# Performance work log

Hardware: AMD Instinct MI355X
Metric: run time of the kernel (lower is better)

The kernel has to match this reference:

```python
import jax, jax.numpy as jnp
import numpy as np
from jax import lax

N = 31      # perfect binary tree, root = node 0, children of i are 2i+1, 2i+2
CH = 10     # hidden channels (out_channel)
S = 8       # hidden spatial size = h_list // 4


def conv3d(x, w, b=None, pad=1):
    out = lax.conv_general_dilated(
        x, w, window_strides=(1, 1, 1), padding=[(pad, pad)] * 3,
        dimension_numbers=('NCDHW', 'OIDHW', 'NCDHW'))
    if b is not None:
        out = out + b[None, :, None, None, None]
    return out


def maxpool2(x):
    return lax.reduce_window(x, -jnp.inf, lax.max, (1, 1, 2, 2, 2), (1, 1, 2, 2, 2), 'VALID')


def up2(x):  # nearest-neighbor upsample x2 on D,H,W
    return jnp.repeat(jnp.repeat(jnp.repeat(x, 2, axis=2), 2, axis=3), 2, axis=4)


def setup_inputs() -> dict:
    key = jax.random.key(0)
    ks = iter(jax.random.split(key, 32))
    r = lambda shape, s=0.1: jax.random.normal(next(ks), shape, dtype=jnp.float32) * s
    inp = {
        'data': jax.random.normal(next(ks), (N, 1, 32, 32, 32), dtype=jnp.float32),
        'h0': jnp.zeros((N, CH, S, S, S), jnp.float32),
        'c0': jnp.zeros((N, CH, S, S, S), jnp.float32),
        'e1a_w': r((16, 1, 3, 3, 3)), 'e1a_b': jnp.zeros((16,), jnp.float32),
        'e1b_w': r((16, 16, 3, 3, 3)), 'e1b_b': jnp.zeros((16,), jnp.float32),
        'e2a_w': r((32, 16, 3, 3, 3)), 'e2a_b': jnp.zeros((32,), jnp.float32),
        'e2b_w': r((20, 32, 3, 3, 3)), 'e2b_b': jnp.zeros((20,), jnp.float32),
        'd2a_w': r((20, 30, 3, 3, 3)), 'd2a_b': jnp.zeros((20,), jnp.float32),
        'd2b_w': r((32, 20, 3, 3, 3)), 'd2b_b': jnp.zeros((32,), jnp.float32),
        'd1a_w': r((16, 48, 3, 3, 3)), 'd1a_b': jnp.zeros((16,), jnp.float32),
        'd1b_w': r((16, 16, 3, 3, 3)), 'd1b_b': jnp.zeros((16,), jnp.float32),
        'd1c_w': r((1, 16, 1, 1, 1)), 'd1c_b': jnp.zeros((1,), jnp.float32),
        'w_iou': r((30, 20, 3, 3, 3)),
        'u_iou': r((30, 10, 3, 3, 3)),
        'u_f': r((10, 10, 3, 3, 3)),
        'b_iou': jnp.zeros((30, S, S, S), jnp.float32),
    }
    return inp


def reference(data, h0, c0, e1a_w, e1a_b, e1b_w, e1b_b, e2a_w, e2a_b, e2b_w, e2b_b,
              d2a_w, d2a_b, d2b_w, d2b_b, d1a_w, d1a_b, d1b_w, d1b_b, d1c_w, d1c_b,
              w_iou, u_iou, u_f, b_iou):
    relu = jax.nn.relu
    # ---- Encoder ----
    x0 = relu(conv3d(relu(conv3d(data, e1a_w, e1a_b)), e1b_w, e1b_b))   # [N,16,32,32,32]
    x = maxpool2(x0)
    x1 = relu(conv3d(relu(conv3d(x, e2a_w, e2a_b)), e2b_w, e2b_b))      # [N,20,16,16,16]
    x = maxpool2(x1)                                                    # [N,20,8,8,8]
    Wx = conv3d(x, w_iou)                                               # [N,30,8,8,8]

    h_all = jnp.zeros((N, CH, S, S, S), Wx.dtype)
    c_all = jnp.zeros((N, CH, S, S, S), Wx.dtype)

    def apply_node(iou, c_in):
        i, o, u = jnp.split(iou + b_iou, 3, axis=1)
        c = jax.nn.sigmoid(i) * jnp.tanh(u) + c_in
        h = jax.nn.sigmoid(o) * jnp.tanh(c)
        return h, c

    # ---- leaves (no children): iou = W_iou(x), c term = initial c0 ----
    leaf = np.arange(N // 2, N)
    h, c = apply_node(Wx[leaf], c0[leaf])
    h_all = h_all.at[leaf].set(h)
    c_all = c_all.at[leaf].set(c)

    # ---- internal levels, bottom-up (topological propagation) ----
    depth = int(np.log2(N + 1))  # 5
    for lvl in range(depth - 2, -1, -1):
        idx = np.arange(2 ** lvl - 1, 2 ** (lvl + 1) - 1)
        ch = np.stack([2 * idx + 1, 2 * idx + 2], axis=1)  # [P,2] children indices
        P = idx.shape[0]
        h_ch = h_all[ch]                                   # [P,2,CH,S,S,S]
        c_ch = c_all[ch]
        h_sum = h_ch.sum(axis=1)
        f = jax.nn.sigmoid(conv3d(h_ch.reshape(P * 2, CH, S, S, S), u_f)).reshape(h_ch.shape)
        c_red = (f * c_ch).sum(axis=1)
        iou = conv3d(h_sum, u_iou)  # NOTE: overwrites W_iou(x) for internal nodes (as in source)
        h, c = apply_node(iou, c_red)
        h_all = h_all.at[idx].set(h)
        c_all = c_all.at[idx].set(c)

    # ---- Decoder (Dropout = identity in eval) ----
    y = up2(h_all)                      # [N,10,16,16,16]
    y = jnp.concatenate([y, x1], axis=1)  # 30 ch
    y = relu(conv3d(y, d2a_w, d2a_b))
    y = relu(conv3d(y, d2b_w, d2b_b))   # 32 ch
    y = up2(y)
    y = jnp.concatenate([y, x0], axis=1)  # 48 ch
    y = relu(conv3d(y, d1a_w, d1a_b))
    y = relu(conv3d(y, d1b_w, d1b_b))
    y = conv3d(y, d1c_w, d1c_b, pad=0)  # [N,1,32,32,32]
    return y
```

## Files before the change

### kernel.cpp

```cpp
#include <hip/hip_runtime.h>
#include <math.h>

typedef _Float16 h2 __attribute__((ext_vector_type(2)));
typedef _Float16 half4_t __attribute__((ext_vector_type(4)));
typedef float f32x4 __attribute__((ext_vector_type(4)));

__device__ inline h2 uph(unsigned u) { return __builtin_bit_cast(h2, u); }
__device__ inline unsigned pkh(float a, float b) {
    return __builtin_bit_cast(unsigned, __builtin_amdgcn_cvt_pkrtz(a, b));
}
__device__ inline float sigf(float x) { return 1.f / (1.f + expf(-x)); }

__global__ __launch_bounds__(256) void repackw(
    const float* __restrict__ src, _Float16* __restrict__ dst,
    int CIw, int CO, int NCH, int total)
{
    int t = blockIdx.x * 256 + threadIdx.x;
    if (t >= total) return;
    int cip = t & 15, co = (t >> 4) & 15, r = t >> 8;
    int tap = r % 27, rc = r / 27;
    int chunk = rc % NCH, slab = rc / NCH;
    int slot_l = ((cip >> 2) - (co >> 2)) & 3;
    int gci = chunk * 16 + slot_l * 4 + (cip & 3);
    int gco = slab * 16 + co;
    float v = 0.f;
    if (gci < CIw && gco < CO) v = src[((size_t)gco * CIw + gci) * 27 + tap];
    dst[t] = (_Float16)v;
}

template<int NCH, int UPP, int UP2, int S2, int CO, int CO2, int D, bool FUSE>
__global__ __launch_bounds__(256) void conv3m(
    const _Float16* __restrict__ up, const _Float16* __restrict__ src,
    const _Float16* __restrict__ bwg, const float* __restrict__ bias,
    _Float16* __restrict__ out, const float* __restrict__ w1c,
    const float* __restrict__ b1c, float* __restrict__ out32)
{
    constexpr int ROWS = (D == 32) ? 10 : 18;
    constexpr int COLS = (D == 32) ? 34 : 18;
    constexpr int DH   = D / 2;
    constexpr int NG   = 3 * ROWS * COLS * 2;
    constexpr int ITERS = (NG + 255) / 256;

    __shared__ __align__(16) _Float16 win[3 * ROWS * COLS * 16];
    __shared__ __align__(16) _Float16 bw[6912];

    const int tid  = threadIdx.x;
    const int lane = tid & 63;
    const int wv   = tid >> 6;
    const int l16  = lane & 15;
    const int quad = lane >> 4;

    int n, d, h0;
    if (D == 32) { h0 = (blockIdx.x & 3) * 8; d = (blockIdx.x >> 2) & 31; n = blockIdx.x >> 7; }
    else         { h0 = 0; d = blockIdx.x & 15; n = blockIdx.x >> 4; }

    const int slab = blockIdx.y;
    const int cob  = slab * 16;
    const int co   = cob + l16;

    size_t baseU[ITERS], baseS[ITERS];
    int dA[ITERS], dB[ITERS];
    bool vld[ITERS];
#pragma unroll
    for (int it = 0; it < ITERS; ++it) {
        int t = tid + it * 256;
        vld[it] = false; dA[it] = 0; dB[it] = 0; baseU[it] = 0; baseS[it] = 0;
        if (t < NG) {
            int g   = t & 1;
            int idx = t >> 1;
            int cc  = idx % COLS;
            int rr  = idx / COLS;
            int hh  = rr % ROWS;
            int dp  = rr / ROWS;
            int zd = d - 1 + dp, zh = h0 + hh - 1, zw = cc - 1;
            vld[it] = (unsigned)zd < (unsigned)D && (unsigned)zh < (unsigned)D &&
                      (unsigned)zw < (unsigned)D;
            int rot  = (cc >> 2) & 3;
            int cell = (rr * COLS + cc) * 16;
            dA[it] = cell + (((2 * g + rot) & 3) << 2);
            dB[it] = cell + (((2 * g + 1 + rot) & 3) << 2);
            if (vld[it]) {
                if (UPP > 0)
                    baseU[it] = ((((size_t)n * DH + (zd >> 1)) * DH + (zh >> 1)) * DH
                                 + (zw >> 1)) * UP2 + g * 8;
                baseS[it] = ((((size_t)n * D + zd) * D + zh) * D + zw) * S2 + g * 8;
            }
        }
    }

    f32x4 acc[4];
    {
        float b0 = (co < CO) ? bias[co] : 0.f;
#pragma unroll
        for (int i = 0; i < 4; ++i) acc[i] = f32x4{b0, b0, b0, b0};
    }

    const int brot = ((quad + (l16 >> 2)) & 3) << 2;

    uint4 preA[ITERS];
    uint4 preB[4];

    auto loadA = [&](int cib) {
        const int cb = cib * 16;
        const bool isup = (UPP > 0) && (cb < UPP);
#pragma unroll
        for (int it = 0; it < ITERS; ++it) {
            int t = tid + it * 256;
            uint4 v = uint4{0u, 0u, 0u, 0u};
            if (t < NG && vld[it]) {
                const _Float16* pp = isup ? (up + baseU[it] + cb)
                                          : (src + baseS[it] + (cb - UPP));
                v = *(const uint4*)pp;
            }
            preA[it] = v;
        }
    };
    auto loadB = [&](int cib) {
        const uint4* bsrc = (const uint4*)(bwg + (size_t)(slab * NCH + cib) * 6912);
#pragma unroll
        for (int it = 0; it < 4; ++it) {
            int t = tid + it * 256;
            preB[it] = (t < 864) ? bsrc[t] : uint4{0u, 0u, 0u, 0u};
        }
    };

    loadA(0);
    loadB(0);

#pragma unroll
    for (int cib = 0; cib < NCH; ++cib) {
        if (cib) __syncthreads();
#pragma unroll
        for (int it = 0; it < 4; ++it) {
            int t = tid + it * 256;
            if (t < 864) ((uint4*)bw)[t] = preB[it];
        }
#pragma unroll
        for (int it = 0; it < ITERS; ++it) {
            int t = tid + it * 256;
            if (t < NG) {
                *(uint2*)&win[dA[it]] = make_uint2(preA[it].x, preA[it].y);
                *(uint2*)&win[dB[it]] = make_uint2(preA[it].z, preA[it].w);
            }
        }
        if (cib + 1 < NCH) { loadA(cib + 1); loadB(cib + 1); }
        __syncthreads();

#pragma unroll
        for (int kd = 0; kd < 3; ++kd) {
#pragma unroll
            for (int kw = 0; kw < 3; ++kw) {
                half4_t bf[3];
#pragma unroll
                for (int kh = 0; kh < 3; ++kh)
                    bf[kh] = *(const half4_t*)&bw[((kd * 3 + kh) * 3 + kw) * 256 + l16 * 16 + brot];
                if (D == 32) {
                    half4_t af[2][4];
#pragma unroll
                    for (int p = 0; p < 2; ++p) {
                        const int ww = p * 16 + l16 + kw;
                        const int arot = ((quad + (ww >> 2)) & 3) << 2;
#pragma unroll
                        for (int rr = 0; rr < 4; ++rr) {
                            const int row = kd * ROWS + wv * 2 + rr;
                            af[p][rr] = *(const half4_t*)&win[(row * COLS + ww) * 16 + arot];
                        }
                    }
#pragma unroll
                    for (int kh = 0; kh < 3; ++kh)
#pragma unroll
                        for (int i = 0; i < 4; ++i)
                            acc[i] = __builtin_amdgcn_mfma_f32_16x16x16f16(
                                af[i & 1][(i >> 1) + kh], bf[kh], acc[i], 0, 0, 0);
                } else {
                    half4_t af[6];
                    const int ww = l16 + kw;
                    const int arot = ((quad + (ww >> 2)) & 3) << 2;
#pragma unroll
                    for (int rr = 0; rr < 6; ++rr) {
                        const int row = kd * ROWS + wv * 4 + rr;
                        af[rr] = *(const half4_t*)&win[(row * COLS + ww) * 16 + arot];
                    }
#pragma unroll
                    for (int kh = 0; kh < 3; ++kh)
#pragma unroll
                        for (int i = 0; i < 4; ++i)
                            acc[i] = __builtin_amdgcn_mfma_f32_16x16x16f16(
                                af[i + kh], bf[kh], acc[i], 0, 0, 0);
                }
            }
        }
    }

    if (FUSE) {
        const float wc = w1c[l16];
        const float bb = b1c[0];
#pragma unroll
        for (int i = 0; i < 4; ++i) {
            const int h = h0 + wv * 2 + (i >> 1);
            const int wb0 = (i & 1) * 16;
#pragma unroll
            for (int r = 0; r < 4; ++r) {
                float v = fmaxf(acc[i][r], 0.f) * wc;
                v += __shfl_xor(v, 1);
                v += __shfl_xor(v, 2);
                v += __shfl_xor(v, 4);
                v += __shfl_xor(v, 8);
                if (l16 == 0) {
                    const int w = wb0 + quad * 4 + r;
                    out32[(((size_t)n * 32 + d) * 32 + h) * 32 + w] = v + bb;
                }
            }
        }
    } else if (co < CO) {
#pragma unroll
        for (int i = 0; i < 4; ++i) {
            int h, wb0;
            if (D == 32) { h = h0 + wv * 2 + (i >> 1); wb0 = (i & 1) * 16; }
            else         { h = wv * 4 + i;             wb0 = 0; }
#pragma unroll
            for (int r = 0; r < 4; ++r) {
                const int w = wb0 + quad * 4 + r;
                size_t sp = (((size_t)n * D + d) * D + h) * D + w;
                out[sp * CO2 + co] = (_Float16)fmaxf(acc[i][r], 0.f);
            }
        }
    }
}

__global__ __launch_bounds__(256) void conv3e1a(
    const float* __restrict__ src, const float* __restrict__ wgt,
    const float* __restrict__ bias, _Float16* __restrict__ out)
{
    __shared__ float sw[27 * 16];
    const int tid = threadIdx.x;
    const int wq = tid % 8;
    const int h  = (tid / 8) % 32;
    const int w0 = wq * 4;
    const int n  = blockIdx.x / 32;
    const int d  = blockIdx.x % 32;

    for (int t = tid; t < 27 * 16; t += 256) {
        int co = t % 16, tap = t / 16;
        sw[t] = wgt[(size_t)co * 27 + tap];
    }
    __syncthreads();

    float acc[16][4];
#pragma unroll
    for (int co = 0; co < 16; ++co) {
        float b0 = bias[co];
        acc[co][0] = b0; acc[co][1] = b0; acc[co][2] = b0; acc[co][3] = b0;
    }

#pragma unroll
    for (int kd = 0; kd < 3; ++kd) {
        int zd = d + kd - 1;
        if ((unsigned)zd >= 32u) continue;
#pragma unroll
        for (int kh = 0; kh < 3; ++kh) {
            int zh = h + kh - 1;
            if ((unsigned)zh >= 32u) continue;
            const float* p = src + ((size_t)n * 32 + zd) * 1024 + zh * 32;
            float v[6];
#pragma unroll
            for (int j = 0; j < 6; ++j) {
                int zw = w0 - 1 + j;
                v[j] = ((unsigned)zw < 32u) ? p[zw] : 0.f;
            }
            const float* swp = &sw[(kd * 9 + kh * 3) * 16];
#pragma unroll
            for (int kw = 0; kw < 3; ++kw)
#pragma unroll
                for (int co = 0; co < 16; ++co)
#pragma unroll
                    for (int j = 0; j < 4; ++j)
                        acc[co][j] = fmaf(v[kw + j], swp[kw * 16 + co], acc[co][j]);
        }
    }

#pragma unroll
    for (int j = 0; j < 4; ++j) {
        unsigned u[8];
#pragma unroll
        for (int cp = 0; cp < 8; ++cp)
            u[cp] = pkh(fmaxf(acc[2 * cp][j], 0.f), fmaxf(acc[2 * cp + 1][j], 0.f));
        _Float16* base = out + ((((size_t)n * 32 + d) * 32 + h) * 32 + (w0 + j)) * 16;
        *(uint4*)base       = make_uint4(u[0], u[1], u[2], u[3]);
        *(uint4*)(base + 8) = make_uint4(u[4], u[5], u[6], u[7]);
    }
}

__global__ __launch_bounds__(256) void maxpool16(
    const unsigned* __restrict__ in, unsigned* __restrict__ out, int total)
{
    int t = blockIdx.x * 256 + threadIdx.x;
    if (t >= total) return;
    int cp = t & 7, w = (t >> 3) & 15, h = (t >> 7) & 15, d = (t >> 11) & 15, n = t >> 15;
    float m0 = -1e30f, m1 = -1e30f;
#pragma unroll
    for (int a = 0; a < 2; ++a)
#pragma unroll
        for (int b = 0; b < 2; ++b)
#pragma unroll
            for (int c = 0; c < 2; ++c) {
                size_t sp = (((size_t)n * 32 + 2 * d + a) * 32 + 2 * h + b) * 32 + 2 * w + c;
                h2 x = uph(in[sp * 8 + cp]);
                m0 = fmaxf(m0, (float)x.x);
                m1 = fmaxf(m1, (float)x.y);
            }
    out[(((size_t)(n * 16 + d) * 16 + h) * 16 + w) * 8 + cp] = pkh(m0, m1);
}

__global__ __launch_bounds__(256) void poolx1(
    const unsigned* __restrict__ x1u, unsigned* __restrict__ out, int total)
{
    int t = blockIdx.x * 256 + threadIdx.x;
    if (t >= total) return;
    int cp = t & 15, s = (t >> 4) & 511, n = t >> 13;
    int w = s & 7, h = (s >> 3) & 7, d = s >> 6;
    unsigned o = 0u;
    if (cp < 10) {
        float m0 = -1e30f, m1 = -1e30f;
#pragma unroll
        for (int a = 0; a < 2; ++a)
#pragma unroll
            for (int b = 0; b < 2; ++b)
#pragma unroll
                for (int c = 0; c < 2; ++c) {
                    size_t sp = (((size_t)n * 16 + 2 * d + a) * 16 + 2 * h + b) * 16 + 2 * w + c;
                    h2 x = uph(x1u[sp * 16 + cp]);
                    m0 = fmaxf(m0, (float)x.x);
                    m1 = fmaxf(m1, (float)x.y);
                }
        o = pkh(m0, m1);
    }
    out[((size_t)n * 512 + s) * 16 + cp] = o;
}

__global__ __launch_bounds__(256) void catk(
    const unsigned* __restrict__ h_allu, const unsigned* __restrict__ x1u,
    unsigned* __restrict__ cat1u, int total)
{
    int t = blockIdx.x * 256 + threadIdx.x;
    if (t >= total) return;
    int cp = t & 15, ww = (t >> 4) & 15, hh = (t >> 8) & 15, dd = (t >> 12) & 15, n = t >> 16;
    unsigned v = 0u;
    if (cp < 5) {
        int sph = (dd >> 1) * 64 + (hh >> 1) * 8 + (ww >> 1);
        v = h_allu[((size_t)n * 512 + sph) * 8 + cp];
    } else if (cp < 15) {
        v = x1u[((((size_t)n * 16 + dd) * 16 + hh) * 16 + ww) * 16 + (cp - 5)];
    }
    cat1u[t] = v;
}

__global__ __launch_bounds__(256) void treeleafM(
    const _Float16* __restrict__ xp2, const _Float16* __restrict__ bwio,
    const float* __restrict__ b_iou, const float* __restrict__ c0,
    _Float16* __restrict__ h_all, _Float16* __restrict__ c_all)
{
    __shared__ __align__(16) _Float16 buf[16384];
    __shared__ __align__(16) _Float16 bw[13824];
    const int tid = threadIdx.x, lane = tid & 63, wv = tid >> 6;
    const int l16 = lane & 15, quad = lane >> 4;
    const int node = 15 + blockIdx.x;
    const _Float16* xb = xp2 + (size_t)node * 512 * 32;
    const int brot = ((quad + (l16 >> 2)) & 3) << 2;

    int base[8];
#pragma unroll
    for (int i = 0; i < 8; ++i) {
        int s = (wv * 8 + i) * 16 + l16;
        base[i] = ((s >> 6) * 10 + ((s >> 3) & 7)) * 10 + (s & 7);
    }

    f32x4 acc[2][8];
#pragma unroll
    for (int sl = 0; sl < 2; ++sl)
#pragma unroll
        for (int i = 0; i < 8; ++i) acc[sl][i] = f32x4{0.f, 0.f, 0.f, 0.f};

    for (int ck = 0; ck < 2; ++ck) {
        if (ck) __syncthreads();
        {
            const uint4* s0 = (const uint4*)(bwio + (size_t)(0 * 2 + ck) * 6912);
            const uint4* s1 = (const uint4*)(bwio + (size_t)(1 * 2 + ck) * 6912);
#pragma unroll
            for (int it = 0; it < 4; ++it) {
                int t = tid + it * 256;
                if (t < 864) { ((uint4*)bw)[t] = s0[t]; ((uint4*)(bw + 6912))[t] = s1[t]; }
            }
        }
#pragma unroll
        for (int it = 0; it < 8; ++it) {
            int t = tid + it * 256;
            if (t < 2000) {
                int g = t & 1, c = t >> 1;
                int zw = c % 10, r = c / 10, zh = r % 10, zd = r / 10;
                int d = zd - 1, h = zh - 1, w = zw - 1;
                uint4 v = uint4{0u, 0u, 0u, 0u};
                if ((unsigned)d < 8u && (unsigned)h < 8u && (unsigned)w < 8u)
                    v = *(const uint4*)(xb + ((d * 8 + h) * 8 + w) * 32 + ck * 16 + g * 8);
                int rot = (c >> 2) & 3;
                *(uint2*)&buf[c * 16 + (((2 * g + rot) & 3) << 2)]     = make_uint2(v.x, v.y);
                *(uint2*)&buf[c * 16 + (((2 * g + 1 + rot) & 3) << 2)] = make_uint2(v.z, v.w);
            }
        }
        __syncthreads();

        for (int kd = 0; kd < 3; ++kd)
        for (int kh = 0; kh < 3; ++kh)
#pragma unroll
        for (int kw = 0; kw < 3; ++kw) {
            int tap = (kd * 3 + kh) * 3 + kw, toff = kd * 100 + kh * 10 + kw;
            half4_t bf0 = *(const half4_t*)&bw[tap * 256 + l16 * 16 + brot];
            half4_t bf1 = *(const half4_t*)&bw[6912 + tap * 256 + l16 * 16 + brot];
#pragma unroll
            for (int i = 0; i < 8; ++i) {
                int cell = base[i] + toff;
                int arot = ((quad + ((cell >> 2) & 3)) & 3) << 2;
                half4_t af = *(const half4_t*)&buf[cell * 16 + arot];
                acc[0][i] = __builtin_amdgcn_mfma_f32_16x16x16f16(af, bf0, acc[0][i], 0, 0, 0);
                acc[1][i] = __builtin_amdgcn_mfma_f32_16x16x16f16(af, bf1, acc[1][i], 0, 0, 0);
            }
        }
    }
    __syncthreads();
#pragma unroll
    for (int sl = 0; sl < 2; ++sl)
#pragma unroll
        for (int i = 0; i < 8; ++i)
#pragma unroll
            for (int r = 0; r < 4; ++r) {
                int s = (wv * 8 + i) * 16 + quad * 4 + r;
                buf[s * 32 + sl * 16 + l16] = (_Float16)acc[sl][i][r];
            }
    __syncthreads();
    for (int sl2 = 0; sl2 < 2; ++sl2) {
        int s = tid + sl2 * 256;
        const uint4* ip = (const uint4*)&buf[s * 32];
        uint4 q0 = ip[0], q1 = ip[1], q2 = ip[2], q3 = ip[3];
        unsigned uw[16] = {q0.x, q0.y, q0.z, q0.w, q1.x, q1.y, q1.z, q1.w,
                           q2.x, q2.y, q2.z, q2.w, q3.x, q3.y, q3.z, q3.w};
        float io[32];
#pragma unroll
        for (int k = 0; k < 16; ++k) { h2 p = uph(uw[k]); io[2 * k] = (float)p.x; io[2 * k + 1] = (float)p.y; }
        unsigned hp[8], cp[8];
#pragma unroll
        for (int q = 0; q < 5; ++q) {
            float hn[2], cn[2];
#pragma unroll
            for (int e = 0; e < 2; ++e) {
                int chn = 2 * q + e;
                float iv = io[chn]      + b_iou[(size_t)chn * 512 + s];
                float ov = io[10 + chn] + b_iou[(size_t)(10 + chn) * 512 + s];
                float uv = io[20 + chn] + b_iou[(size_t)(20 + chn) * 512 + s];
                float cin = c0[((size_t)node * 10 + chn) * 512 + s];
                cn[e] = sigf(iv) * tanhf(uv) + cin;
                hn[e] = sigf(ov) * tanhf(cn[e]);
            }
            hp[q] = pkh(hn[0], hn[1]);
            cp[q] = pkh(cn[0], cn[1]);
        }
        hp[5] = hp[6] = hp[7] = 0u; cp[5] = cp[6] = cp[7] = 0u;
        uint4* ho = (uint4*)(h_all + ((size_t)node * 512 + s) * 16);
        uint4* co_ = (uint4*)(c_all + ((size_t)node * 512 + s) * 16);
        ho[0] = make_uint4(hp[0], hp[1], hp[2], hp[3]);
        ho[1] = make_uint4(hp[4], hp[5], hp[6], hp[7]);
        co_[0] = make_uint4(cp[0], cp[1], cp[2], cp[3]);
        co_[1] = make_uint4(cp[4], cp[5], cp[6], cp[7]);
    }
}

__global__ __launch_bounds__(256) void treelevelM(
    const _Float16* __restrict__ bwuf, const _Float16* __restrict__ bwui,
    const float* __restrict__ b_iou,
    _Float16* __restrict__ h_all, _Float16* __restrict__ c_all,
    int pb, int cb)
{
    __shared__ __align__(16) _Float16 buf[16384];
    __shared__ __align__(16) _Float16 bw[13824];
    const int tid = threadIdx.x, lane = tid & 63, wv = tid >> 6;
    const int l16 = lane & 15, quad = lane >> 4;
    const int node = pb + blockIdx.x;
    const int c0n = cb + 2 * blockIdx.x;
    const int brot = ((quad + (l16 >> 2)) & 3) << 2;

    int base[8];
#pragma unroll
    for (int i = 0; i < 8; ++i) {
        int s = (wv * 8 + i) * 16 + l16;
        base[i] = ((s >> 6) * 10 + ((s >> 3) & 7)) * 10 + (s & 7);
    }

    float cred[10][2];
#pragma unroll
    for (int c = 0; c < 10; ++c) cred[c][0] = cred[c][1] = 0.f;

#pragma unroll
    for (int it = 0; it < 4; ++it) {
        int t = tid + it * 256;
        if (t < 864) ((uint4*)bw)[t] = ((const uint4*)bwuf)[t];
    }

    for (int e = 0; e < 2; ++e) {
        const _Float16* hb = h_all + (size_t)(c0n + e) * 512 * 16;
        if (e) __syncthreads();
#pragma unroll
        for (int it = 0; it < 8; ++it) {
            int t = tid + it * 256;
            if (t < 2000) {
                int g = t & 1, c = t >> 1;
                int zw = c % 10, r = c / 10, zh = r % 10, zd = r / 10;
                int d = zd - 1, h = zh - 1, w = zw - 1;
                uint4 v = uint4{0u, 0u, 0u, 0u};
                if ((unsigned)d < 8u && (unsigned)h < 8u && (unsigned)w < 8u)
                    v = *(const uint4*)(hb + ((d * 8 + h) * 8 + w) * 16 + g * 8);
                int rot = (c >> 2) & 3;
                *(uint2*)&buf[c * 16 + (((2 * g + rot) & 3) << 2)]     = make_uint2(v.x, v.y);
                *(uint2*)&buf[c * 16 + (((2 * g + 1 + rot) & 3) << 2)] = make_uint2(v.z, v.w);
            }
        }
        __syncthreads();
        f32x4 accf[8];
#pragma unroll
        for (int i = 0; i < 8; ++i) accf[i] = f32x4{0.f, 0.f, 0.f, 0.f};
        for (int kd = 0; kd < 3; ++kd)
        for (int kh = 0; kh < 3; ++kh)
#pragma unroll
        for (int kw = 0; kw < 3; ++kw) {
            int tap = (kd * 3 + kh) * 3 + kw, toff = kd * 100 + kh * 10 + kw;
            half4_t bf = *(const half4_t*)&bw[tap * 256 + l16 * 16 + brot];
#pragma unroll
            for (int i = 0; i < 8; ++i) {
                int cell = base[i] + toff;
                int arot = ((quad + ((cell >> 2) & 3)) & 3) << 2;
                half4_t af = *(const half4_t*)&buf[cell * 16 + arot];
                accf[i] = __builtin_amdgcn_mfma_f32_16x16x16f16(af, bf, accf[i], 0, 0, 0);
            }
        }
        __syncthreads();
#pragma unroll
        for (int i = 0; i < 8; ++i)
#pragma unroll
            for (int r = 0; r < 4; ++r) {
                int s = (wv * 8 + i) * 16 + quad * 4 + r;
                buf[s * 16 + l16] = (_Float16)accf[i][r];
            }
        __syncthreads();
        for (int sl2 = 0; sl2 < 2; ++sl2) {
            int s = tid + sl2 * 256;
            const uint4* fp_ = (const uint4*)&buf[s * 16];
            uint4 f0 = fp_[0], f1 = fp_[1];
            unsigned fw[8] = {f0.x, f0.y, f0.z, f0.w, f1.x, f1.y, f1.z, f1.w};
            const uint4* cc = (const uint4*)(c_all + ((size_t)(c0n + e) * 512 + s) * 16);
            uint4 c0v = cc[0], c1v = cc[1];
            unsigned cw[8] = {c0v.x, c0v.y, c0v.z, c0v.w, c1v.x, c1v.y, c1v.z, c1v.w};
#pragma unroll
            for (int q = 0; q < 5; ++q) {
                h2 fv = uph(fw[q]); h2 cv = uph(cw[q]);
                cred[2 * q][sl2]     += sigf((float)fv.x) * (float)cv.x;
                cred[2 * q + 1][sl2] += sigf((float)fv.y) * (float)cv.y;
            }
        }
    }
    __syncthreads();
#pragma unroll
    for (int it = 0; it < 7; ++it) {
        int t = tid + it * 256;
        if (t < 1728) ((uint4*)bw)[t] = ((const uint4*)bwui)[t];
    }
    {
        const _Float16* h0b = h_all + (size_t)c0n * 512 * 16;
        const _Float16* h1b = h_all + (size_t)(c0n + 1) * 512 * 16;
#pragma unroll
        for (int it = 0; it < 8; ++it) {
            int t = tid + it * 256;
            if (t < 2000) {
                int g = t & 1, c = t >> 1;
                int zw = c % 10, r = c / 10, zh = r % 10, zd = r / 10;
                int d = zd - 1, h = zh - 1, w = zw - 1;
                uint4 v = uint4{0u, 0u, 0u, 0u};
                if ((unsigned)d < 8u && (unsigned)h < 8u && (unsigned)w < 8u) {
                    size_t off = ((d * 8 + h) * 8 + w) * 16 + g * 8;
                    uint4 a = *(const uint4*)(h0b + off);
                    uint4 b = *(const uint4*)(h1b + off);
                    unsigned* av = &a.x; unsigned* bv = &b.x; unsigned* vv = &v.x;
#pragma unroll
                    for (int k = 0; k < 4; ++k) {
                        h2 x = uph(av[k]); h2 y = uph(bv[k]);
                        vv[k] = pkh((float)x.x + (float)y.x, (float)x.y + (float)y.y);
                    }
                }
                int rot = (c >> 2) & 3;
                *(uint2*)&buf[c * 16 + (((2 * g + rot) & 3) << 2)]     = make_uint2(v.x, v.y);
                *(uint2*)&buf[c * 16 + (((2 * g + 1 + rot) & 3) << 2)] = make_uint2(v.z, v.w);
            }
        }
    }
    __syncthreads();
    f32x4 acc[2][8];
#pragma unroll
    for (int sl = 0; sl < 2; ++sl)
#pragma unroll
        for (int i = 0; i < 8; ++i) acc[sl][i] = f32x4{0.f, 0.f, 0.f, 0.f};
    for (int kd = 0; kd < 3; ++kd)
    for (int kh = 0; kh < 3; ++kh)
#pragma unroll
    for (int kw = 0; kw < 3; ++kw) {
        int tap = (kd * 3 + kh) * 3 + kw, toff = kd * 100 + kh * 10 + kw;
        half4_t bf0 = *(const half4_t*)&bw[tap * 256 + l16 * 16 + brot];
        half4_t bf1 = *(const half4_t*)&bw[6912 + tap * 256 + l16 * 16 + brot];
#pragma unroll
        for (int i = 0; i < 8; ++i) {
            int cell = base[i] + toff;
            int arot = ((quad + ((cell >> 2) & 3)) & 3) << 2;
            half4_t af = *(const half4_t*)&buf[cell * 16 + arot];
            acc[0][i] = __builtin_amdgcn_mfma_f32_16x16x16f16(af, bf0, acc[0][i], 0, 0, 0);
            acc[1][i] = __builtin_amdgcn_mfma_f32_16x16x16f16(af, bf1, acc[1][i], 0, 0, 0);
        }
    }
    __syncthreads();
#pragma unroll
    for (int sl = 0; sl < 2; ++sl)
#pragma unroll
        for (int i = 0; i < 8; ++i)
#pragma unroll
            for (int r = 0; r < 4; ++r) {
                int s = (wv * 8 + i) * 16 + quad * 4 + r;
                buf[s * 32 + sl * 16 + l16] = (_Float16)acc[sl][i][r];
            }
    __syncthreads();
    for (int sl2 = 0; sl2 < 2; ++sl2) {
        int s = tid + sl2 * 256;
        const uint4* ip = (const uint4*)&buf[s * 32];
        uint4 q0 = ip[0], q1 = ip[1], q2 = ip[2], q3 = ip[3];
        unsigned uw[16] = {q0.x, q0.y, q0.z, q0.w, q1.x, q1.y, q1.z, q1.w,
                           q2.x, q2.y, q2.z, q2.w, q3.x, q3.y, q3.z, q3.w};
        float io[32];
#pragma unroll
        for (int k = 0; k < 16; ++k) { h2 p = uph(uw[k]); io[2 * k] = (float)p.x; io[2 * k + 1] = (float)p.y; }
        unsigned hp[8], cp[8];
#pragma unroll
        for (int q = 0; q < 5; ++q) {
            float hn[2], cn[2];
#pragma unroll
            for (int e = 0; e < 2; ++e) {
                int chn = 2 * q + e;
                float iv = io[chn]      + b_iou[(size_t)chn * 512 + s];
                float ov = io[10 + chn] + b_iou[(size_t)(10 + chn) * 512 + s];
                float uv = io[20 + chn] + b_iou[(size_t)(20 + chn) * 512 + s];
                cn[e] = sigf(iv) * tanhf(uv) + cred[chn][sl2];
                hn[e] = sigf(ov) * tanhf(cn[e]);
            }
            hp[q] = pkh(hn[0], hn[1]);
            cp[q] = pkh(cn[0], cn[1]);
        }
        hp[5] = hp[6] = hp[7] = 0u; cp[5] = cp[6] = cp[7] = 0u;
        uint4* ho = (uint4*)(h_all + ((size_t)node * 512 + s) * 16);
        uint4* co_ = (uint4*)(c_all + ((size_t)node * 512 + s) * 16);
        ho[0] = make_uint4(hp[0], hp[1], hp[2], hp[3]);
        ho[1] = make_uint4(hp[4], hp[5], hp[6], hp[7]);
        co_[0] = make_uint4(cp[0], cp[1], cp[2], cp[3]);
        co_[1] = make_uint4(cp[4], cp[5], cp[6], cp[7]);
    }
}

extern "C" void kernel_launch(void* const* d_in, const int* in_sizes, int n_in,
                              void* d_out, int out_size, void* d_ws, size_t ws_size,
                              hipStream_t stream)
{
    const float* data  = (const float*)d_in[0];
    const float* c0    = (const float*)d_in[2];
    const float* e1a_w = (const float*)d_in[3];  const float* e1a_b = (const float*)d_in[4];
    const float* e1b_w = (const float*)d_in[5];  const float* e1b_b = (const float*)d_in[6];
    const float* e2a_w = (const float*)d_in[7];  const float* e2a_b = (const float*)d_in[8];
    const float* e2b_w = (const float*)d_in[9];  const float* e2b_b = (const float*)d_in[10];
    const float* d2a_w = (const float*)d_in[11]; const float* d2a_b = (const float*)d_in[12];
    const float* d2b_w = (const float*)d_in[13]; const float* d2b_b = (const float*)d_in[14];
    const float* d1a_w = (const float*)d_in[15]; const float* d1a_b = (const float*)d_in[16];
    const float* d1b_w = (const float*)d_in[17]; const float* d1b_b = (const float*)d_in[18];
    const float* d1c_w = (const float*)d_in[19]; const float* d1c_b = (const float*)d_in[20];
    const float* w_iou = (const float*)d_in[21];
    const float* u_iou = (const float*)d_in[22];
    const float* u_f   = (const float*)d_in[23];
    const float* b_iou = (const float*)d_in[24];

    unsigned* ws = (unsigned*)d_ws;
    size_t o = 0;
    unsigned* t1u   = ws + o; o += 8126464;
    unsigned* x0u   = ws + o; o += 8126464;
    unsigned* xpu   = ws + o; o += 1015808;
    unsigned* t2u   = ws + o; o += 2031616;
    unsigned* x1u   = ws + o; o += 2031616;
    unsigned* cat1u = ws + o; o += 2031616;
    unsigned* y2u   = ws + o; o += 2031616;
    unsigned* xp2u  = ws + o; o += 253952;
    unsigned* h_allu= ws + o; o += 126976;
    unsigned* c_allu= ws + o; o += 126976;
    unsigned* bwgu  = ws + o; o += 89856;
    (void)ws_size; (void)in_sizes; (void)n_in; (void)out_size;

    _Float16* t1h  = (_Float16*)t1u;
    _Float16* x0h  = (_Float16*)x0u;
    _Float16* xph  = (_Float16*)xpu;
    _Float16* t2h  = (_Float16*)t2u;
    _Float16* x1h  = (_Float16*)x1u;
    _Float16* cath = (_Float16*)cat1u;
    _Float16* y2h  = (_Float16*)y2u;
    _Float16* xp2h = (_Float16*)xp2u;
    _Float16* h_allh = (_Float16*)h_allu;
    _Float16* c_allh = (_Float16*)c_allu;
    _Float16* t3h  = t2h;
    _Float16* t4h  = t1h;
    _Float16* bwg  = (_Float16*)bwgu;

    _Float16* b_e1b = bwg;
    _Float16* b_e2a = bwg + 6912;
    _Float16* b_e2b = bwg + 20736;
    _Float16* b_d2a = bwg + 48384;
    _Float16* b_d2b = bwg + 76032;
    _Float16* b_d1a = bwg + 103680;
    _Float16* b_d1b = bwg + 124416;
    _Float16* b_wio = bwg + 131328;
    _Float16* b_uio = bwg + 158976;
    _Float16* b_uf  = bwg + 172800;

    dim3 b256(256);

    repackw<<<dim3(27),  b256, 0, stream>>>(e1b_w, b_e1b, 16, 16, 1, 6912);
    repackw<<<dim3(54),  b256, 0, stream>>>(e2a_w, b_e2a, 16, 32, 1, 13824);
    repackw<<<dim3(108), b256, 0, stream>>>(e2b_w, b_e2b, 32, 20, 2, 27648);
    repackw<<<dim3(108), b256, 0, stream>>>(d2a_w, b_d2a, 30, 20, 2, 27648);
    repackw<<<dim3(108), b256, 0, stream>>>(d2b_w, b_d2b, 20, 32, 2, 27648);
    repackw<<<dim3(81),  b256, 0, stream>>>(d1a_w, b_d1a, 48, 16, 3, 20736);
    repackw<<<dim3(27),  b256, 0, stream>>>(d1b_w, b_d1b, 16, 16, 1, 6912);
    repackw<<<dim3(108), b256, 0, stream>>>(w_iou, b_wio, 20, 30, 2, 27648);
    repackw<<<dim3(54),  b256, 0, stream>>>(u_iou, b_uio, 10, 30, 1, 13824);
    repackw<<<dim3(27),  b256, 0, stream>>>(u_f,   b_uf,  10, 10, 1, 6912);

    conv3e1a<<<dim3(992), b256, 0, stream>>>(data, e1a_w, e1a_b, t1h);
    conv3m<1, 0, 0, 16, 16, 16, 32, false><<<dim3(3968, 1), b256, 0, stream>>>(
        nullptr, t1h, b_e1b, e1b_b, x0h, nullptr, nullptr, nullptr);
    maxpool16<<<dim3(3968), b256, 0, stream>>>(x0u, xpu, 1015808);
    conv3m<1, 0, 0, 16, 32, 32, 16, false><<<dim3(496, 2), b256, 0, stream>>>(
        nullptr, xph, b_e2a, e2a_b, t2h, nullptr, nullptr, nullptr);
    conv3m<2, 0, 0, 32, 20, 32, 16, false><<<dim3(496, 2), b256, 0, stream>>>(
        nullptr, t2h, b_e2b, e2b_b, x1h, nullptr, nullptr, nullptr);
    poolx1<<<dim3(992), b256, 0, stream>>>(x1u, xp2u, 253952);

    treeleafM<<<dim3(16), b256, 0, stream>>>(xp2h, b_wio, b_iou, c0, h_allh, c_allh);
    for (int lvl = 3; lvl >= 0; --lvl) {
        int P = 1 << lvl;
        treelevelM<<<dim3(P), b256, 0, stream>>>(
            b_uf, b_uio, b_iou, h_allh, c_allh, P - 1, 2 * P - 1);
    }

    catk<<<dim3(7936), b256, 0, stream>>>(h_allu, x1u, cat1u, 2031616);
    conv3m<2, 0, 0, 32, 20, 32, 16, false><<<dim3(496, 2), b256, 0, stream>>>(
        nullptr, cath, b_d2a, d2a_b, t3h, nullptr, nullptr, nullptr);
    conv3m<2, 0, 0, 32, 32, 32, 16, false><<<dim3(496, 2), b256, 0, stream>>>(
        nullptr, t3h, b_d2b, d2b_b, y2h, nullptr, nullptr, nullptr);
    conv3m<3, 32, 32, 16, 16, 16, 32, false><<<dim3(3968, 1), b256, 0, stream>>>(
        y2h, x0h, b_d1a, d1a_b, t4h, nullptr, nullptr, nullptr);
    conv3m<1, 0, 0, 16, 16, 16, 32, true><<<dim3(3968, 1), b256, 0, stream>>>(
        nullptr, t4h, b_d1b, d1b_b, nullptr, d1c_w, d1c_b, (float*)d_out);
}
```

Measured before the change: 552.2 us.

## Enlarge conv tiles, compute both output-channel slabs per block, merge weight repacks

Result: no change. 556.0 us (+0.7%).

```diff
diff --git a/kernel.cpp b/kernel.cpp
--- a/kernel.cpp
+++ b/kernel.cpp
@@ -11,13 +11,29 @@
 }
 __device__ inline float sigf(float x) { return 1.f / (1.f + expf(-x)); }
 
-__global__ __launch_bounds__(256) void repackw(
-    const float* __restrict__ src, _Float16* __restrict__ dst,
-    int CIw, int CO, int NCH, int total)
+__global__ __launch_bounds__(256) void repackall(
+    const float* __restrict__ s0, const float* __restrict__ s1,
+    const float* __restrict__ s2, const float* __restrict__ s3,
+    const float* __restrict__ s4, const float* __restrict__ s5,
+    const float* __restrict__ s6, const float* __restrict__ s7,
+    const float* __restrict__ s8, const float* __restrict__ s9,
+    _Float16* __restrict__ dst)
 {
     int t = blockIdx.x * 256 + threadIdx.x;
-    if (t >= total) return;
-    int cip = t & 15, co = (t >> 4) & 15, r = t >> 8;
+    if (t >= 179712) return;
+    const int offs[11] = {0, 6912, 20736, 48384, 76032, 103680, 124416,
+                          131328, 158976, 172800, 179712};
+    const int ciwA[10] = {16, 16, 32, 30, 20, 48, 16, 20, 10, 10};
+    const int coA[10]  = {16, 32, 20, 20, 32, 16, 16, 30, 30, 10};
+    const int nchA[10] = {1, 1, 2, 2, 2, 3, 1, 2, 1, 1};
+    int seg = 0;
+    while (t >= offs[seg + 1]) ++seg;
+    int lt = t - offs[seg];
+    const float* src = seg == 0 ? s0 : seg == 1 ? s1 : seg == 2 ? s2 :
+                       seg == 3 ? s3 : seg == 4 ? s4 : seg == 5 ? s5 :
+                       seg == 6 ? s6 : seg == 7 ? s7 : seg == 8 ? s8 : s9;
+    int CIw = ciwA[seg], CO = coA[seg], NCH = nchA[seg];
+    int cip = lt & 15, co = (lt >> 4) & 15, r = lt >> 8;
     int tap = r % 27, rc = r / 27;
     int chunk = rc % NCH, slab = rc / NCH;
     int slot_l = ((cip >> 2) - (co >> 2)) & 3;
@@ -28,20 +44,18 @@
     dst[t] = (_Float16)v;
 }
 
-template<int NCH, int UPP, int UP2, int S2, int CO, int CO2, int D, bool FUSE>
-__global__ __launch_bounds__(256) void conv3m(
+template<int NCH, int UPP, int UP2, int S2, bool FUSE>
+__global__ __launch_bounds__(256) void conv3m32(
     const _Float16* __restrict__ up, const _Float16* __restrict__ src,
     const _Float16* __restrict__ bwg, const float* __restrict__ bias,
     _Float16* __restrict__ out, const float* __restrict__ w1c,
     const float* __restrict__ b1c, float* __restrict__ out32)
 {
-    constexpr int ROWS = (D == 32) ? 10 : 18;
-    constexpr int COLS = (D == 32) ? 34 : 18;
-    constexpr int DH   = D / 2;
-    constexpr int NG   = 3 * ROWS * COLS * 2;
-    constexpr int ITERS = (NG + 255) / 256;
-
-    __shared__ __align__(16) _Float16 win[3 * ROWS * COLS * 16];
+    constexpr int ROWS = 18, COLS = 34;
+    constexpr int CELLS = 3 * ROWS * COLS;
+    constexpr int ITERS = 8;
+
+    __shared__ __align__(16) _Float16 win[CELLS * 16];
     __shared__ __align__(16) _Float16 bw[6912];
 
     const int tid  = threadIdx.x;
@@ -50,73 +64,59 @@
     const int l16  = lane & 15;
     const int quad = lane >> 4;
 
-    int n, d, h0;
-    if (D == 32) { h0 = (blockIdx.x & 3) * 8; d = (blockIdx.x >> 2) & 31; n = blockIdx.x >> 7; }
-    else         { h0 = 0; d = blockIdx.x & 15; n = blockIdx.x >> 4; }
-
-    const int slab = blockIdx.y;
-    const int cob  = slab * 16;
-    const int co   = cob + l16;
-
-    size_t baseU[ITERS], baseS[ITERS];
-    int dA[ITERS], dB[ITERS];
+    const int h0 = (blockIdx.x & 1) * 16;
+    const int d  = (blockIdx.x >> 1) & 31;
+    const int n  = blockIdx.x >> 6;
+
+    unsigned baseS[ITERS], baseU[ITERS], pk[ITERS];
     bool vld[ITERS];
 #pragma unroll
     for (int it = 0; it < ITERS; ++it) {
         int t = tid + it * 256;
-        vld[it] = false; dA[it] = 0; dB[it] = 0; baseU[it] = 0; baseS[it] = 0;
-        if (t < NG) {
-            int g   = t & 1;
-            int idx = t >> 1;
-            int cc  = idx % COLS;
-            int rr  = idx / COLS;
-            int hh  = rr % ROWS;
-            int dp  = rr / ROWS;
+        vld[it] = false; baseS[it] = 0; baseU[it] = 0; pk[it] = 0;
+        if (t < CELLS) {
+            int cc = t % COLS, rr = t / COLS;
+            int hh = rr % ROWS, dp = rr / ROWS;
             int zd = d - 1 + dp, zh = h0 + hh - 1, zw = cc - 1;
-            vld[it] = (unsigned)zd < (unsigned)D && (unsigned)zh < (unsigned)D &&
-                      (unsigned)zw < (unsigned)D;
-            int rot  = (cc >> 2) & 3;
-            int cell = (rr * COLS + cc) * 16;
-            dA[it] = cell + (((2 * g + rot) & 3) << 2);
-            dB[it] = cell + (((2 * g + 1 + rot) & 3) << 2);
+            vld[it] = (unsigned)zd < 32u && (unsigned)zh < 32u && (unsigned)zw < 32u;
+            pk[it] = (unsigned)(t * 16) | ((unsigned)((cc >> 2) & 3) << 28);
             if (vld[it]) {
+                baseS[it] = (unsigned)((((n * 32 + zd) * 32 + zh) * 32 + zw) * S2);
                 if (UPP > 0)
-                    baseU[it] = ((((size_t)n * DH + (zd >> 1)) * DH + (zh >> 1)) * DH
-                                 + (zw >> 1)) * UP2 + g * 8;
-                baseS[it] = ((((size_t)n * D + zd) * D + zh) * D + zw) * S2 + g * 8;
-            }
-        }
-    }
-
-    f32x4 acc[4];
+                    baseU[it] = (unsigned)((((n * 16 + (zd >> 1)) * 16 + (zh >> 1)) * 16
+                                            + (zw >> 1)) * UP2);
+            }
+        }
+    }
+
+    f32x4 acc[8];
     {
-        float b0 = (co < CO) ? bias[co] : 0.f;
-#pragma unroll
-        for (int i = 0; i < 4; ++i) acc[i] = f32x4{b0, b0, b0, b0};
-    }
-
+        float b0 = bias[l16];
+#pragma unroll
+        for (int i = 0; i < 8; ++i) acc[i] = f32x4{b0, b0, b0, b0};
+    }
     const int brot = ((quad + (l16 >> 2)) & 3) << 2;
 
-    uint4 preA[ITERS];
-    uint4 preB[4];
+    uint4 preA0[ITERS], preA1[ITERS], preB[4];
 
     auto loadA = [&](int cib) {
         const int cb = cib * 16;
         const bool isup = (UPP > 0) && (cb < UPP);
 #pragma unroll
         for (int it = 0; it < ITERS; ++it) {
+            uint4 v0 = uint4{0u, 0u, 0u, 0u}, v1 = v0;
             int t = tid + it * 256;
-            uint4 v = uint4{0u, 0u, 0u, 0u};
-            if (t < NG && vld[it]) {
-                const _Float16* pp = isup ? (up + baseU[it] + cb)
-                                          : (src + baseS[it] + (cb - UPP));
-                v = *(const uint4*)pp;
-            }
-            preA[it] = v;
+            if (t < CELLS && vld[it]) {
+                const _Float16* p = isup ? (up + baseU[it] + cb)
+                                         : (src + baseS[it] + (cb - UPP));
+                v0 = *(const uint4*)p;
+                v1 = *(const uint4*)(p + 8);
+            }
+            preA0[it] = v0; preA1[it] = v1;
         }
     };
     auto loadB = [&](int cib) {
-        const uint4* bsrc = (const uint4*)(bwg + (size_t)(slab * NCH + cib) * 6912);
+        const uint4* bsrc = (const uint4*)(bwg + (size_t)cib * 6912);
 #pragma unroll
         for (int it = 0; it < 4; ++it) {
             int t = tid + it * 256;
@@ -138,9 +138,13 @@
 #pragma unroll
         for (int it = 0; it < ITERS; ++it) {
             int t = tid + it * 256;
-            if (t < NG) {
-                *(uint2*)&win[dA[it]] = make_uint2(preA[it].x, preA[it].y);
-                *(uint2*)&win[dB[it]] = make_uint2(preA[it].z, preA[it].w);
+            if (t < CELLS) {
+                int cell = pk[it] & 0x0FFFFFFF;
+                int rot  = pk[it] >> 28;
+                *(uint2*)&win[cell + (((rot + 0) & 3) << 2)] = make_uint2(preA0[it].x, preA0[it].y);
+                *(uint2*)&win[cell + (((rot + 1) & 3) << 2)] = make_uint2(preA0[it].z, preA0[it].w);
+                *(uint2*)&win[cell + (((rot + 2) & 3) << 2)] = make_uint2(preA1[it].x, preA1[it].y);
+                *(uint2*)&win[cell + (((rot + 3) & 3) << 2)] = make_uint2(preA1[it].z, preA1[it].w);
             }
         }
         if (cib + 1 < NCH) { loadA(cib + 1); loadB(cib + 1); }
@@ -154,40 +158,25 @@
 #pragma unroll
                 for (int kh = 0; kh < 3; ++kh)
                     bf[kh] = *(const half4_t*)&bw[((kd * 3 + kh) * 3 + kw) * 256 + l16 * 16 + brot];
-                if (D == 32) {
-                    half4_t af[2][4];
-#pragma unroll
-                    for (int p = 0; p < 2; ++p) {
-                        const int ww = p * 16 + l16 + kw;
-                        const int arot = ((quad + (ww >> 2)) & 3) << 2;
-#pragma unroll
-                        for (int rr = 0; rr < 4; ++rr) {
-                            const int row = kd * ROWS + wv * 2 + rr;
-                            af[p][rr] = *(const half4_t*)&win[(row * COLS + ww) * 16 + arot];
-                        }
-                    }
-#pragma unroll
-                    for (int kh = 0; kh < 3; ++kh)
-#pragma unroll
-                        for (int i = 0; i < 4; ++i)
-                            acc[i] = __builtin_amdgcn_mfma_f32_16x16x16f16(
-                                af[i & 1][(i >> 1) + kh], bf[kh], acc[i], 0, 0, 0);
-                } else {
-                    half4_t af[6];
-                    const int ww = l16 + kw;
+                half4_t af[2][6];
+#pragma unroll
+                for (int p = 0; p < 2; ++p) {
+                    const int ww = p * 16 + l16 + kw;
                     const int arot = ((quad + (ww >> 2)) & 3) << 2;
 #pragma unroll
                     for (int rr = 0; rr < 6; ++rr) {
                         const int row = kd * ROWS + wv * 4 + rr;
-                        af[rr] = *(const half4_t*)&win[(row * COLS + ww) * 16 + arot];
+                        af[p][rr] = *(const half4_t*)&win[(row * COLS + ww) * 16 + arot];
                     }
-#pragma unroll
-                    for (int kh = 0; kh < 3; ++kh)
-#pragma unroll
-                        for (int i = 0; i < 4; ++i)
-                            acc[i] = __builtin_amdgcn_mfma_f32_16x16x16f16(
-                                af[i + kh], bf[kh], acc[i], 0, 0, 0);
                 }
+#pragma unroll
+                for (int kh = 0; kh < 3; ++kh)
+#pragma unroll
+                    for (int j = 0; j < 4; ++j)
+#pragma unroll
+                        for (int p = 0; p < 2; ++p)
+                            acc[j * 2 + p] = __builtin_amdgcn_mfma_f32_16x16x16f16(
+                                af[p][j + kh], bf[kh], acc[j * 2 + p], 0, 0, 0);
             }
         }
     }
@@ -196,8 +185,8 @@
         const float wc = w1c[l16];
         const float bb = b1c[0];
 #pragma unroll
-        for (int i = 0; i < 4; ++i) {
-            const int h = h0 + wv * 2 + (i >> 1);
+        for (int i = 0; i < 8; ++i) {
+            const int h = h0 + wv * 4 + (i >> 1);
             const int wb0 = (i & 1) * 16;
 #pragma unroll
             for (int r = 0; r < 4; ++r) {
@@ -212,17 +201,166 @@
                 }
             }
         }
-    } else if (co < CO) {
-#pragma unroll
-        for (int i = 0; i < 4; ++i) {
-            int h, wb0;
-            if (D == 32) { h = h0 + wv * 2 + (i >> 1); wb0 = (i & 1) * 16; }
-            else         { h = wv * 4 + i;             wb0 = 0; }
+    } else {
+#pragma unroll
+        for (int i = 0; i < 8; ++i) {
+            const int h = h0 + wv * 4 + (i >> 1);
+            const int wb0 = (i & 1) * 16;
 #pragma unroll
             for (int r = 0; r < 4; ++r) {
                 const int w = wb0 + quad * 4 + r;
-                size_t sp = (((size_t)n * D + d) * D + h) * D + w;
-                out[sp * CO2 + co] = (_Float16)fmaxf(acc[i][r], 0.f);
+                size_t sp = (((size_t)n * 32 + d) * 32 + h) * 32 + w;
+                out[sp * 16 + l16] = (_Float16)fmaxf(acc[i][r], 0.f);
+            }
+        }
+    }
+}
+
+template<int NCH, int NSLAB, int S2, int CO>
+__global__ __launch_bounds__(256) void conv3m16(
+    const _Float16* __restrict__ src, const _Float16* __restrict__ bwg,
+    const float* __restrict__ bias, _Float16* __restrict__ out)
+{
+    constexpr int ROWS = 18, COLS = 18;
+    constexpr int CELLS = 3 * ROWS * COLS;
+    constexpr int ITERS = 4;
+
+    __shared__ __align__(16) _Float16 win[CELLS * 16];
+    __shared__ __align__(16) _Float16 bw[NSLAB * 6912];
+
+    const int tid  = threadIdx.x;
+    const int lane = tid & 63;
+    const int wv   = tid >> 6;
+    const int l16  = lane & 15;
+    const int quad = lane >> 4;
+
+    const int d = blockIdx.x & 15;
+    const int n = blockIdx.x >> 4;
+
+    unsigned baseS[ITERS], pk[ITERS];
+    bool vld[ITERS];
+#pragma unroll
+    for (int it = 0; it < ITERS; ++it) {
+        int t = tid + it * 256;
+        vld[it] = false; baseS[it] = 0; pk[it] = 0;
+        if (t < CELLS) {
+            int cc = t % COLS, rr = t / COLS;
+            int hh = rr % ROWS, dp = rr / ROWS;
+            int zd = d - 1 + dp, zh = hh - 1, zw = cc - 1;
+            vld[it] = (unsigned)zd < 16u && (unsigned)zh < 16u && (unsigned)zw < 16u;
+            pk[it] = (unsigned)(t * 16) | ((unsigned)((cc >> 2) & 3) << 28);
+            if (vld[it])
+                baseS[it] = (unsigned)((((n * 16 + zd) * 16 + zh) * 16 + zw) * S2);
+        }
+    }
+
+    f32x4 acc[NSLAB][4];
+#pragma unroll
+    for (int s = 0; s < NSLAB; ++s) {
+        int cg = s * 16 + l16;
+        float b0 = (cg < CO) ? bias[cg] : 0.f;
+#pragma unroll
+        for (int i = 0; i < 4; ++i) acc[s][i] = f32x4{b0, b0, b0, b0};
+    }
+    const int brot = ((quad + (l16 >> 2)) & 3) << 2;
+
+    uint4 preA0[ITERS], preA1[ITERS], preB[NSLAB][4];
+
+    auto loadA = [&](int cib) {
+        const int cb = cib * 16;
+#pragma unroll
+        for (int it = 0; it < ITERS; ++it) {
+            uint4 v0 = uint4{0u, 0u, 0u, 0u}, v1 = v0;
+            int t = tid + it * 256;
+            if (t < CELLS && vld[it]) {
+                const _Float16* p = src + baseS[it] + cb;
+                v0 = *(const uint4*)p;
+                v1 = *(const uint4*)(p + 8);
+            }
+            preA0[it] = v0; preA1[it] = v1;
+        }
+    };
+    auto loadB = [&](int cib) {
+#pragma unroll
+        for (int s = 0; s < NSLAB; ++s) {
+            const uint4* bsrc = (const uint4*)(bwg + (size_t)(s * NCH + cib) * 6912);
+#pragma unroll
+            for (int it = 0; it < 4; ++it) {
+                int t = tid + it * 256;
+                preB[s][it] = (t < 864) ? bsrc[t] : uint4{0u, 0u, 0u, 0u};
+            }
+        }
+    };
+
+    loadA(0);
+    loadB(0);
+
+#pragma unroll
+    for (int cib = 0; cib < NCH; ++cib) {
+        if (cib) __syncthreads();
+#pragma unroll
+        for (int s = 0; s < NSLAB; ++s)
+#pragma unroll
+            for (int it = 0; it < 4; ++it) {
+                int t = tid + it * 256;
+                if (t < 864) ((uint4*)(bw + s * 6912))[t] = preB[s][it];
+            }
+#pragma unroll
+        for (int it = 0; it < ITERS; ++it) {
+            int t = tid + it * 256;
+            if (t < CELLS) {
+                int cell = pk[it] & 0x0FFFFFFF;
+                int rot  = pk[it] >> 28;
+                *(uint2*)&win[cell + (((rot + 0) & 3) << 2)] = make_uint2(preA0[it].x, preA0[it].y);
+                *(uint2*)&win[cell + (((rot + 1) & 3) << 2)] = make_uint2(preA0[it].z, preA0[it].w);
+                *(uint2*)&win[cell + (((rot + 2) & 3) << 2)] = make_uint2(preA1[it].x, preA1[it].y);
+                *(uint2*)&win[cell + (((rot + 3) & 3) << 2)] = make_uint2(preA1[it].z, preA1[it].w);
+            }
+        }
+        if (cib + 1 < NCH) { loadA(cib + 1); loadB(cib + 1); }
+        __syncthreads();
+
+#pragma unroll
+        for (int kd = 0; kd < 3; ++kd) {
+#pragma unroll
+            for (int kw = 0; kw < 3; ++kw) {
+                half4_t af[6];
+                const int ww = l16 + kw;
+                const int arot = ((quad + (ww >> 2)) & 3) << 2;
+#pragma unroll
+                for (int rr = 0; rr < 6; ++rr) {
+                    const int row = kd * ROWS + wv * 4 + rr;
+                    af[rr] = *(const half4_t*)&win[(row * COLS + ww) * 16 + arot];
+                }
+#pragma unroll
+                for (int kh = 0; kh < 3; ++kh) {
+                    const int tap = (kd * 3 + kh) * 3 + kw;
+#pragma unroll
+                    for (int s = 0; s < NSLAB; ++s) {
+                        half4_t bf = *(const half4_t*)&bw[s * 6912 + tap * 256 + l16 * 16 + brot];
+#pragma unroll
+                        for (int i = 0; i < 4; ++i)
+                            acc[s][i] = __builtin_amdgcn_mfma_f32_16x16x16f16(
+                                af[i + kh], bf, acc[s][i], 0, 0, 0);
+                    }
+                }
+            }
+        }
+    }
+
+#pragma unroll
+    for (int s = 0; s < NSLAB; ++s) {
+        int cg = s * 16 + l16;
+        if (cg < CO) {
+#pragma unroll
+            for (int i = 0; i < 4; ++i) {
+                const int h = wv * 4 + i;
+#pragma unroll
+                for (int r = 0; r < 4; ++r) {
+                    const int w = quad * 4 + r;
+                    size_t sp = (((size_t)n * 16 + d) * 16 + h) * 16 + w;
+                    out[sp * 32 + cg] = (_Float16)fmaxf(acc[s][i][r], 0.f);
+                }
             }
         }
     }
@@ -729,25 +867,15 @@
 
     dim3 b256(256);
 
-    repackw<<<dim3(27),  b256, 0, stream>>>(e1b_w, b_e1b, 16, 16, 1, 6912);
-    repackw<<<dim3(54),  b256, 0, stream>>>(e2a_w, b_e2a, 16, 32, 1, 13824);
-    repackw<<<dim3(108), b256, 0, stream>>>(e2b_w, b_e2b, 32, 20, 2, 27648);
-    repackw<<<dim3(108), b256, 0, stream>>>(d2a_w, b_d2a, 30, 20, 2, 27648);
-    repackw<<<dim3(108), b256, 0, stream>>>(d2b_w, b_d2b, 20, 32, 2, 27648);
-    repackw<<<dim3(81),  b256, 0, stream>>>(d1a_w, b_d1a, 48, 16, 3, 20736);
-    repackw<<<dim3(27),  b256, 0, stream>>>(d1b_w, b_d1b, 16, 16, 1, 6912);
-    repackw<<<dim3(108), b256, 0, stream>>>(w_iou, b_wio, 20, 30, 2, 27648);
-    repackw<<<dim3(54),  b256, 0, stream>>>(u_iou, b_uio, 10, 30, 1, 13824);
-    repackw<<<dim3(27),  b256, 0, stream>>>(u_f,   b_uf,  10, 10, 1, 6912);
+    repackall<<<dim3(702), b256, 0, stream>>>(
+        e1b_w, e2a_w, e2b_w, d2a_w, d2b_w, d1a_w, d1b_w, w_iou, u_iou, u_f, bwg);
 
     conv3e1a<<<dim3(992), b256, 0, stream>>>(data, e1a_w, e1a_b, t1h);
-    conv3m<1, 0, 0, 16, 16, 16, 32, false><<<dim3(3968, 1), b256, 0, stream>>>(
+    conv3m32<1, 0, 0, 16, false><<<dim3(1984), b256, 0, stream>>>(
         nullptr, t1h, b_e1b, e1b_b, x0h, nullptr, nullptr, nullptr);
     maxpool16<<<dim3(3968), b256, 0, stream>>>(x0u, xpu, 1015808);
-    conv3m<1, 0, 0, 16, 32, 32, 16, false><<<dim3(496, 2), b256, 0, stream>>>(
-        nullptr, xph, b_e2a, e2a_b, t2h, nullptr, nullptr, nullptr);
-    conv3m<2, 0, 0, 32, 20, 32, 16, false><<<dim3(496, 2), b256, 0, stream>>>(
-        nullptr, t2h, b_e2b, e2b_b, x1h, nullptr, nullptr, nullptr);
+    conv3m16<1, 2, 16, 32><<<dim3(496), b256, 0, stream>>>(xph, b_e2a, e2a_b, t2h);
+    conv3m16<2, 2, 32, 20><<<dim3(496), b256, 0, stream>>>(t2h, b_e2b, e2b_b, x1h);
     poolx1<<<dim3(992), b256, 0, stream>>>(x1u, xp2u, 253952);
 
     treeleafM<<<dim3(16), b256, 0, stream>>>(xp2h, b_wio, b_iou, c0, h_allh, c_allh);
@@ -758,12 +886,10 @@
     }
 
     catk<<<dim3(7936), b256, 0, stream>>>(h_allu, x1u, cat1u, 2031616);
-    conv3m<2, 0, 0, 32, 20, 32, 16, false><<<dim3(496, 2), b256, 0, stream>>>(
-        nullptr, cath, b_d2a, d2a_b, t3h, nullptr, nullptr, nullptr);
-    conv3m<2, 0, 0, 32, 32, 32, 16, false><<<dim3(496, 2), b256, 0, stream>>>(
-        nullptr, t3h, b_d2b, d2b_b, y2h, nullptr, nullptr, nullptr);
-    conv3m<3, 32, 32, 16, 16, 16, 32, false><<<dim3(3968, 1), b256, 0, stream>>>(
+    conv3m16<2, 2, 32, 20><<<dim3(496), b256, 0, stream>>>(cath, b_d2a, d2a_b, t3h);
+    conv3m16<2, 2, 32, 32><<<dim3(496), b256, 0, stream>>>(t3h, b_d2b, d2b_b, y2h);
+    conv3m32<3, 32, 32, 16, false><<<dim3(1984), b256, 0, stream>>>(
         y2h, x0h, b_d1a, d1a_b, t4h, nullptr, nullptr, nullptr);
-    conv3m<1, 0, 0, 16, 16, 16, 32, true><<<dim3(3968, 1), b256, 0, stream>>>(
+    conv3m32<1, 0, 0, 16, true><<<dim3(1984), b256, 0, stream>>>(
         nullptr, t4h, b_d1b, d1b_b, nullptr, d1c_w, d1c_b, (float*)d_out);
 }
```
